# Kernel optimization log

Hardware: AMD Instinct MI355X
Metric: run time of the kernel (lower is better)

The kernel has to match this reference:

```python
import jax, jax.numpy as jnp
import numpy as np

W_CUB = 0.1
W_CD = 1.0
W_EXT = 0.01
W_SPS = 0.01
THRED = 24.0
COS_EPS = 1e-4

# cube face buffers (6 faces x 3 coords)
MASK_PROJECT = jnp.array([[0,1,1],[0,1,1],[1,0,1],[1,0,1],[1,1,0],[1,1,0]], jnp.float32)
MASK_PLANE   = jnp.array([[1,0,0],[1,0,0],[0,1,0],[0,1,0],[0,0,1],[0,0,1]], jnp.float32)
CUBE_NORMAL  = jnp.array([[-1,0,0],[1,0,0],[0,-1,0],[0,1,0],[0,0,-1],[0,0,1]], jnp.float32)
# torch repeat(...,3,...) of [[-1,-1,-1],[1,1,1]] tiles it -> [c0,c1,c0,c1,c0,c1]
CUBE_PLANES6 = jnp.tile(jnp.array([[-1.,-1.,-1.],[1.,1.,1.]], jnp.float32), (3,1))


def setup_inputs():
    B, P, N, S = 4, 24, 3072, 128
    key = jax.random.key(0)
    ks = jax.random.split(key, 8)
    pc_inver = jax.random.normal(ks[0], (B, P, N, 3), jnp.float32)
    normals_inver = jax.random.normal(ks[1], (B, P, N, 3), jnp.float32)
    scale = jax.random.uniform(ks[2], (B, P, 3), jnp.float32) * 0.9 + 0.1
    shape = jax.random.uniform(ks[3], (B, P, 2), jnp.float32) * 1.3 + 0.2
    exist = jax.random.uniform(ks[4], (B, P, 1), jnp.float32) * 0.98 + 0.01
    assign_matrix = jax.nn.softmax(jax.random.normal(ks[5], (B, N, P), jnp.float32), axis=-1)
    etas = jax.random.uniform(ks[6], (B, P, S), jnp.float32, minval=-jnp.pi/2, maxval=jnp.pi/2)
    omegas = jax.random.uniform(ks[7], (B, P, S), jnp.float32, minval=-jnp.pi, maxval=jnp.pi)
    return dict(pc_inver=pc_inver, normals_inver=normals_inver, scale=scale,
                shape=shape, exist=exist, assign_matrix=assign_matrix,
                etas=etas, omegas=omegas)


def _fexp(x, p):
    return jnp.sign(x) * jnp.abs(x) ** p


def _sample_sq_points(scale, eps, etas, omegas):
    # scale (B,P,3), eps (B,P,2), etas/omegas (B,P,S) -> (B,P,S,3)
    etas = jnp.where(etas == 0, 1e-6, etas)
    omegas = jnp.where(omegas == 0, 1e-6, omegas)
    a1, a2, a3 = scale[..., 0:1], scale[..., 1:2], scale[..., 2:3]
    e1, e2 = eps[..., 0:1], eps[..., 1:2]
    ce, se = jnp.cos(etas), jnp.sin(etas)
    co, so = jnp.cos(omegas), jnp.sin(omegas)
    x = a1 * _fexp(ce, e1) * _fexp(co, e2)
    y = a2 * _fexp(ce, e1) * _fexp(so, e2)
    z = a3 * _fexp(se, e1)
    fix = lambda v: (jnp.where(v > 0, 1.0, -1.0)) * jnp.maximum(jnp.abs(v), 1e-6)
    return jnp.stack([fix(x), fix(y), fix(z)], -1)


def _cd_loss(pc_inver, scale, shape, exist, assign_matrix, etas, omegas):
    X = _sample_sq_points(scale, shape, etas, omegas)          # (B,P,S,3)
    diff = X[:, :, :, None, :] - pc_inver[:, :, None, :, :]    # (B,P,S,N,3)
    D = jnp.sum(diff * diff, -1)                               # (B,P,S,N)
    pcl2prim = jnp.min(D, axis=2)                              # (B,P,N)
    pcl_loss = jnp.mean(jnp.sum(jnp.swapaxes(pcl2prim, 1, 2) * assign_matrix, -1))
    prim2pcl = jnp.mean(jnp.min(D, axis=3), axis=-1)           # (B,P)
    e = exist[..., 0]
    prim_loss = jnp.mean(jnp.sum(prim2pcl * e, -1) / (jnp.sum(e, -1) + 1e-6))
    return pcl_loss, prim_loss


def _cuboid_loss(pc_inver, normals_inver, scale, assign_matrix):
    pc = jnp.swapaxes(pc_inver, 1, 2)        # (B,N,P,3)
    nrm = jnp.swapaxes(normals_inver, 1, 2)  # (B,N,P,3)
    n_norm = jnp.maximum(jnp.linalg.norm(nrm, axis=-1, keepdims=True), COS_EPS)
    cos = jnp.einsum('bnpc,fc->bnpf', nrm, CUBE_NORMAL) / n_norm  # ||cube_normal||=1
    idx = jnp.argmax(cos, axis=-1)           # (B,N,P)
    s = scale[:, None, :, None, :]           # (B,1,P,1,3)
    proj = pc[:, :, :, None, :] * MASK_PROJECT + (CUBE_PLANES6 * s) * MASK_PLANE  # (B,N,P,6,3)
    proj = jnp.clip(proj, -s, s)
    proj_sel = jnp.take_along_axis(proj, idx[..., None, None], axis=3)[..., 0, :]  # (B,N,P,3)
    d = jnp.sum((proj_sel - pc) ** 2, -1)    # (B,N,P)
    return jnp.mean(jnp.sum(d * assign_matrix, -1))


def _common_losses(assign_matrix, exist):
    gt = jax.lax.stop_gradient((jnp.sum(assign_matrix, 1) > THRED).astype(jnp.float32))  # (B,P)
    p = exist[..., 0]
    bce = -jnp.mean(gt * jnp.log(p) + (1.0 - gt) * jnp.log1p(-p))
    N = assign_matrix.shape[1]
    sps = jnp.mean(jnp.mean(jnp.sqrt(jnp.sum(assign_matrix, 1) / N + 0.01), -1) ** 2)
    return bce, sps


def reference(pc_inver, normals_inver, scale, shape, exist, assign_matrix, etas, omegas):
    cub = _cuboid_loss(pc_inver, normals_inver, scale, assign_matrix)
    pcl_loss, prim_loss = _cd_loss(pc_inver, scale, shape, exist, assign_matrix, etas, omegas)
    bce, sps = _common_losses(assign_matrix, exist)
    return W_CUB * cub + W_CD * (pcl_loss + prim_loss) + W_EXT * bce + W_SPS * sps
```

## Files before the change

kernel.cpp:

```cpp
#include <hip/hip_runtime.h>
#include <math.h>

#define BB 4
#define PP 24
#define NN 3072
#define SS 128
#define CHUNK 512
#define NSPLIT 6
#define GRID (BB * PP * NSPLIT)
#define FINF 3.4e38f

#define SMIN_F  0
#define SCAL_F  (96 * SS * 8)
#define BPRES_F (SCAL_F + 96 * NSPLIT * 4)
#define CNT_F   (BPRES_F + 96 * 4)

__device__ __forceinline__ float fexp_f(float v, float p) {
    float m = powf(fabsf(v), p);
    float s = (v > 0.f) ? 1.f : ((v < 0.f) ? -1.f : 0.f);
    return s * m;
}
__device__ __forceinline__ float fix_f(float v) {
    return ((v > 0.f) ? 1.f : -1.f) * fmaxf(fabsf(v), 1e-6f);
}
__device__ __forceinline__ float wave_sum(float v) {
    #pragma unroll
    for (int off = 32; off > 0; off >>= 1) v += __shfl_down(v, off);
    return v;
}
__device__ __forceinline__ float aload(const float* p) {
    return __hip_atomic_load(p, __ATOMIC_RELAXED, __HIP_MEMORY_SCOPE_AGENT);
}
__device__ __forceinline__ void astore(float* p, float v) {
    __hip_atomic_store(p, v, __ATOMIC_RELAXED, __HIP_MEMORY_SCOPE_AGENT);
}
__device__ __forceinline__ float cub_dist(float px, float py, float pz,
                                          float nx, float ny, float nz,
                                          float sc0, float sc1, float sc2) {
    float best = -nx; int idx = 0;
    if ( nx > best) { best =  nx; idx = 1; }
    if (-ny > best) { best = -ny; idx = 2; }
    if ( ny > best) { best =  ny; idx = 3; }
    if (-nz > best) { best = -nz; idx = 4; }
    if ( nz > best) { best =  nz; idx = 5; }
    const int c = idx >> 1;
    const float scc = (c == 0) ? sc0 : ((c == 1) ? sc1 : sc2);
    const float fv  = (idx & 1) ? scc : -scc;
    float pr0 = (c == 0) ? fv : fminf(fmaxf(px, -sc0), sc0);
    float pr1 = (c == 1) ? fv : fminf(fmaxf(py, -sc1), sc1);
    float pr2 = (c == 2) ? fv : fminf(fmaxf(pz, -sc2), sc2);
    float d0 = pr0 - px, d1 = pr1 - py, d2 = pr2 - pz;
    return fmaf(d0, d0, fmaf(d1, d1, d2 * d2));
}

__global__ __launch_bounds__(128) void superdec_init(float* __restrict__ ws) {
    const int i = threadIdx.x;
    if (i < 97) ((unsigned*)(ws + CNT_F))[i] = 0u;
}

__global__ __launch_bounds__(256) void superdec_fused(
    const float* __restrict__ pc, const float* __restrict__ nrm,
    const float* __restrict__ scale, const float* __restrict__ shape,
    const float* __restrict__ exist, const float* __restrict__ assign,
    const float* __restrict__ etas, const float* __restrict__ omegas,
    float* __restrict__ ws, float* __restrict__ out)
{
    const int blk   = blockIdx.x;
    const int bp    = blk / NSPLIT;
    const int split = blk % NSPLIT;
    const int b     = bp / PP;
    const int p     = bp % PP;
    const int tid   = threadIdx.x;
    const int n0    = split * CHUNK;
    const int pid   = tid & 127;
    const int q     = tid >> 7;

    __shared__ float4 Xs[SS];
    __shared__ float4 Pts[CHUNK];
    __shared__ float4 dmin2[2][128];
    __shared__ float  red[8 * SS];
    __shared__ float  wsum[6];
    __shared__ unsigned int s_cnt1, s_cnt2;

    const float sc0 = scale[bp * 3 + 0];
    const float sc1 = scale[bp * 3 + 1];
    const float sc2 = scale[bp * 3 + 2];

    const float4* pc4 = (const float4*)(pc + ((size_t)bp * NN + n0) * 3);
    const float4 g0 = pc4[pid * 3 + 0];
    const float4 g1 = pc4[pid * 3 + 1];
    const float4 g2 = pc4[pid * 3 + 2];
    const float px0 = g0.x, py0 = g0.y, pz0 = g0.z;
    const float px1 = g0.w, py1 = g1.x, pz1 = g1.y;
    const float px2 = g1.z, py2 = g1.w, pz2 = g2.x;
    const float px3 = g2.y, py3 = g2.z, pz3 = g2.w;
    const float ps0 = fmaf(px0, px0, fmaf(py0, py0, pz0 * pz0));
    const float ps1 = fmaf(px1, px1, fmaf(py1, py1, pz1 * pz1));
    const float ps2 = fmaf(px2, px2, fmaf(py2, py2, pz2 * pz2));
    const float ps3 = fmaf(px3, px3, fmaf(py3, py3, pz3 * pz3));

    float cub0 = 0.f, cub1 = 0.f, cub2 = 0.f, cub3 = 0.f;
    float am0 = 0.f, am1 = 0.f, am2 = 0.f, am3 = 0.f;

    if (q == 0) {
        {
            const float e1 = shape[bp * 2 + 0];
            const float e2 = shape[bp * 2 + 1];
            float eta = etas[bp * SS + tid];
            float omg = omegas[bp * SS + tid];
            eta = (eta == 0.f) ? 1e-6f : eta;
            omg = (omg == 0.f) ? 1e-6f : omg;
            float ce = cosf(eta), se = sinf(eta);
            float co = cosf(omg), so = sinf(omg);
            float fce = fexp_f(ce, e1);
            float x = fix_f(sc0 * fce * fexp_f(co, e2));
            float y = fix_f(sc1 * fce * fexp_f(so, e2));
            float z = fix_f(sc2 * fexp_f(se, e1));
            float xsq = fmaf(x, x, fmaf(y, y, z * z));
            Xs[tid] = make_float4(-2.f * x, -2.f * y, -2.f * z, xsq);
        }
        Pts[pid * 4 + 0] = make_float4(px0, py0, pz0, ps0);
        Pts[pid * 4 + 1] = make_float4(px1, py1, pz1, ps1);
        Pts[pid * 4 + 2] = make_float4(px2, py2, pz2, ps2);
        Pts[pid * 4 + 3] = make_float4(px3, py3, pz3, ps3);
        const float4* nr4 = (const float4*)(nrm + ((size_t)bp * NN + n0) * 3);
        const float4 h0 = nr4[pid * 3 + 0];
        const float4 h1 = nr4[pid * 3 + 1];
        const float4 h2 = nr4[pid * 3 + 2];
        cub0 = cub_dist(px0, py0, pz0, h0.x, h0.y, h0.z, sc0, sc1, sc2);
        cub1 = cub_dist(px1, py1, pz1, h0.w, h1.x, h1.y, sc0, sc1, sc2);
        cub2 = cub_dist(px2, py2, pz2, h1.z, h1.w, h2.x, sc0, sc1, sc2);
        cub3 = cub_dist(px3, py3, pz3, h2.y, h2.z, h2.w, sc0, sc1, sc2);
        const size_t abase = ((size_t)b * NN + n0 + pid * 4) * PP + p;
        am0 = assign[abase + 0 * PP];
        am1 = assign[abase + 1 * PP];
        am2 = assign[abase + 2 * PP];
        am3 = assign[abase + 3 * PP];
    }
    __syncthreads();

    {
        const int sb = q * 64;
        float m0 = FINF, m1 = FINF, m2 = FINF, m3 = FINF;
        #pragma unroll 4
        for (int s = 0; s < 64; s += 2) {
            float4 xa = Xs[sb + s];
            float4 xb = Xs[sb + s + 1];
            float d;
            d = fmaf(xa.x, px0, fmaf(xa.y, py0, fmaf(xa.z, pz0, xa.w))); m0 = fminf(m0, d);
            d = fmaf(xa.x, px1, fmaf(xa.y, py1, fmaf(xa.z, pz1, xa.w))); m1 = fminf(m1, d);
            d = fmaf(xa.x, px2, fmaf(xa.y, py2, fmaf(xa.z, pz2, xa.w))); m2 = fminf(m2, d);
            d = fmaf(xa.x, px3, fmaf(xa.y, py3, fmaf(xa.z, pz3, xa.w))); m3 = fminf(m3, d);
            d = fmaf(xb.x, px0, fmaf(xb.y, py0, fmaf(xb.z, pz0, xb.w))); m0 = fminf(m0, d);
            d = fmaf(xb.x, px1, fmaf(xb.y, py1, fmaf(xb.z, pz1, xb.w))); m1 = fminf(m1, d);
            d = fmaf(xb.x, px2, fmaf(xb.y, py2, fmaf(xb.z, pz2, xb.w))); m2 = fminf(m2, d);
            d = fmaf(xb.x, px3, fmaf(xb.y, py3, fmaf(xb.z, pz3, xb.w))); m3 = fminf(m3, d);
        }
        dmin2[q][pid] = make_float4(m0, m1, m2, m3);
    }
    __syncthreads();

    if (q == 0) {
        float4 a = dmin2[0][pid];
        float4 c = dmin2[1][pid];
        float d0 = fminf(a.x, c.x) + ps0;
        float d1 = fminf(a.y, c.y) + ps1;
        float d2 = fminf(a.z, c.z) + ps2;
        float d3 = fminf(a.w, c.w) + ps3;
        float acc_pcl = d0 * am0 + d1 * am1 + d2 * am2 + d3 * am3;
        float acc_cub = cub0 * am0 + cub1 * am1 + cub2 * am2 + cub3 * am3;
        float acc_am  = am0 + am1 + am2 + am3;
        float s0 = wave_sum(acc_pcl);
        float s1 = wave_sum(acc_cub);
        float s2 = wave_sum(acc_am);
        const int lane_ = tid & 63, wave = tid >> 6;
        if (lane_ == 0) {
            wsum[wave * 3 + 0] = s0;
            wsum[wave * 3 + 1] = s1;
            wsum[wave * 3 + 2] = s2;
        }
    }

    {
        const int rep = tid >> 5;
        const int sb  = tid & 31;
        const float4 x0 = Xs[sb];
        const float4 x1 = Xs[sb + 32];
        const float4 x2 = Xs[sb + 64];
        const float4 x3 = Xs[sb + 96];
        const int nb = rep * 64;
        float r0 = FINF, r1 = FINF, r2 = FINF, r3 = FINF;
        #pragma unroll 4
        for (int n = 0; n < 64; n += 2) {
            float4 pa = Pts[nb + n];
            float4 pb = Pts[nb + n + 1];
            float d;
            d = fmaf(x0.x, pa.x, fmaf(x0.y, pa.y, fmaf(x0.z, pa.z, pa.w))); r0 = fminf(r0, d);
            d = fmaf(x1.x, pa.x, fmaf(x1.y, pa.y, fmaf(x1.z, pa.z, pa.w))); r1 = fminf(r1, d);
            d = fmaf(x2.x, pa.x, fmaf(x2.y, pa.y, fmaf(x2.z, pa.z, pa.w))); r2 = fminf(r2, d);
            d = fmaf(x3.x, pa.x, fmaf(x3.y, pa.y, fmaf(x3.z, pa.z, pa.w))); r3 = fminf(r3, d);
            d = fmaf(x0.x, pb.x, fmaf(x0.y, pb.y, fmaf(x0.z, pb.z, pb.w))); r0 = fminf(r0, d);
            d = fmaf(x1.x, pb.x, fmaf(x1.y, pb.y, fmaf(x1.z, pb.z, pb.w))); r1 = fminf(r1, d);
            d = fmaf(x2.x, pb.x, fmaf(x2.y, pb.y, fmaf(x2.z, pb.z, pb.w))); r2 = fminf(r2, d);
            d = fmaf(x3.x, pb.x, fmaf(x3.y, pb.y, fmaf(x3.z, pb.z, pb.w))); r3 = fminf(r3, d);
        }
        red[rep * SS + sb +  0] = r0;
        red[rep * SS + sb + 32] = r1;
        red[rep * SS + sb + 64] = r2;
        red[rep * SS + sb + 96] = r3;
    }
    __syncthreads();

    if (tid < SS) {
        float m = red[tid];
        #pragma unroll
        for (int r = 1; r < 8; ++r) m = fminf(m, red[r * SS + tid]);
        astore(ws + SMIN_F + ((bp * SS + tid) << 3) + split, m + Xs[tid].w);
    }
    if (tid == 0) {
        float* sc = ws + SCAL_F + (bp * NSPLIT + split) * 4;
        astore(sc + 0, wsum[0] + wsum[3]);
        astore(sc + 1, wsum[1] + wsum[4]);
        astore(sc + 2, wsum[2] + wsum[5]);
    }

    __syncthreads();
    if (tid == 0) {
        asm volatile("s_waitcnt vmcnt(0)" ::: "memory");
        s_cnt1 = __hip_atomic_fetch_add((unsigned*)(ws + CNT_F) + bp, 1u,
                                        __ATOMIC_RELAXED, __HIP_MEMORY_SCOPE_AGENT);
    }
    __syncthreads();
    if (s_cnt1 != (unsigned)(NSPLIT - 1)) return;

    {
        const int lane = tid & 63;
        if (tid < SS) {
            const float* mb = ws + SMIN_F + ((bp * SS + tid) << 3);
            const float v0 = aload(mb + 0), v1 = aload(mb + 1), v2 = aload(mb + 2);
            const float v3 = aload(mb + 3), v4 = aload(mb + 4), v5 = aload(mb + 5);
            float m = fminf(fminf(fminf(v0, v1), fminf(v2, v3)), fminf(v4, v5));
            float sm = wave_sum(m);
            if (lane == 0) wsum[tid >> 6] = sm;
        } else if (tid < 128 + 18) {
            const int j = tid - 128, sp = j / 3, c = j % 3;
            red[600 + j] = aload(ws + SCAL_F + (bp * NSPLIT + sp) * 4 + c);
        }
        __syncthreads();
        if (tid == 0) {
            const float prim = wsum[0] + wsum[1];
            float pcl = 0.f, cubv = 0.f, cs = 0.f;
            #pragma unroll
            for (int sp = 0; sp < NSPLIT; ++sp) {
                pcl  += red[600 + sp * 3 + 0];
                cubv += red[600 + sp * 3 + 1];
                cs   += red[600 + sp * 3 + 2];
            }
            float* r4 = ws + BPRES_F + bp * 4;
            astore(r4 + 0, prim);
            astore(r4 + 1, pcl);
            astore(r4 + 2, cubv);
            astore(r4 + 3, cs);
            asm volatile("s_waitcnt vmcnt(0)" ::: "memory");
            s_cnt2 = __hip_atomic_fetch_add((unsigned*)(ws + CNT_F) + 96, 1u,
                                            __ATOMIC_RELAXED, __HIP_MEMORY_SCOPE_AGENT);
        }
        __syncthreads();
        if (s_cnt2 != 95u) return;
    }

    if (tid < 96) {
        const float* r4 = ws + BPRES_F + tid * 4;
        const float prim = aload(r4 + 0);
        const float pcl  = aload(r4 + 1);
        const float cubv = aload(r4 + 2);
        const float cs   = aload(r4 + 3);
        const float e  = exist[tid];
        const float gt = (cs > 24.0f) ? 1.f : 0.f;
        red[  0 + tid] = prim;
        red[ 96 + tid] = pcl;
        red[192 + tid] = cubv;
        red[288 + tid] = gt * logf(e) + (1.f - gt) * log1pf(-e);
        red[384 + tid] = e;
        red[480 + tid] = sqrtf(cs / (float)NN + 0.01f);
    }
    __syncthreads();

    if (tid == 0) {
        float pcl_sum = 0.f, cub_sum = 0.f, bce_sum = 0.f, prim_loss = 0.f, sps = 0.f;
        #pragma unroll
        for (int b_ = 0; b_ < BB; ++b_) {
            float pe = 0.f, ee = 0.f, sq = 0.f;
            #pragma unroll
            for (int p_ = 0; p_ < PP; ++p_) {
                const int i = b_ * PP + p_;
                pcl_sum += red[ 96 + i];
                cub_sum += red[192 + i];
                bce_sum += red[288 + i];
                pe += (red[i] / (float)SS) * red[384 + i];
                ee += red[384 + i];
                sq += red[480 + i];
            }
            prim_loss += pe / (ee + 1e-6f);
            float mb = sq / (float)PP;
            sps += mb * mb;
        }
        prim_loss /= (float)BB;
        sps       /= (float)BB;
        float pcl_loss = pcl_sum / (float)(BB * NN);
        float cubf     = cub_sum / (float)(BB * NN);
        float bce      = -bce_sum / (float)(BB * PP);
        out[0] = 0.1f * cubf + 1.0f * (pcl_loss + prim_loss) + 0.01f * bce + 0.01f * sps;
    }
}

extern "C" void kernel_launch(void* const* d_in, const int* in_sizes, int n_in,
                              void* d_out, int out_size, void* d_ws, size_t ws_size,
                              hipStream_t stream) {
    const float* pc     = (const float*)d_in[0];
    const float* nrm    = (const float*)d_in[1];
    const float* scale  = (const float*)d_in[2];
    const float* shape  = (const float*)d_in[3];
    const float* exist  = (const float*)d_in[4];
    const float* assign = (const float*)d_in[5];
    const float* etas   = (const float*)d_in[6];
    const float* omegas = (const float*)d_in[7];
    float* ws  = (float*)d_ws;
    float* out = (float*)d_out;

    superdec_init<<<1, 128, 0, stream>>>(ws);

    superdec_fused<<<GRID, 256, 0, stream>>>(
        pc, nrm, scale, shape, exist, assign, etas, omegas, ws, out);
}
```

Before: 89.23 us.

## Compute each distance once for both Chamfer directions in a fused tile pass

```diff
diff --git a/kernel.cpp b/kernel.cpp
--- a/kernel.cpp
+++ b/kernel.cpp
@@ -72,160 +72,169 @@
     const int p     = bp % PP;
     const int tid   = threadIdx.x;
     const int n0    = split * CHUNK;
-    const int pid   = tid & 127;
-    const int q     = tid >> 7;
+    const int pg    = tid & 63;
+    const int sg    = tid >> 6;
 
     __shared__ float4 Xs[SS];
-    __shared__ float4 Pts[CHUNK];
-    __shared__ float4 dmin2[2][128];
-    __shared__ float  red[8 * SS];
+    __shared__ float  s_red[4][32][68];
+    __shared__ float4 dminL[4][64][2];
+    __shared__ float4 cubam[128][2];
+    __shared__ float  red[1024];
     __shared__ float  wsum[6];
-    __shared__ unsigned int s_cnt1, s_cnt2;
+    __shared__ unsigned s_cnt1, s_cnt2;
 
     const float sc0 = scale[bp * 3 + 0];
     const float sc1 = scale[bp * 3 + 1];
     const float sc2 = scale[bp * 3 + 2];
 
     const float4* pc4 = (const float4*)(pc + ((size_t)bp * NN + n0) * 3);
-    const float4 g0 = pc4[pid * 3 + 0];
-    const float4 g1 = pc4[pid * 3 + 1];
-    const float4 g2 = pc4[pid * 3 + 2];
-    const float px0 = g0.x, py0 = g0.y, pz0 = g0.z;
-    const float px1 = g0.w, py1 = g1.x, pz1 = g1.y;
-    const float px2 = g1.z, py2 = g1.w, pz2 = g2.x;
-    const float px3 = g2.y, py3 = g2.z, pz3 = g2.w;
-    const float ps0 = fmaf(px0, px0, fmaf(py0, py0, pz0 * pz0));
-    const float ps1 = fmaf(px1, px1, fmaf(py1, py1, pz1 * pz1));
-    const float ps2 = fmaf(px2, px2, fmaf(py2, py2, pz2 * pz2));
-    const float ps3 = fmaf(px3, px3, fmaf(py3, py3, pz3 * pz3));
-
-    float cub0 = 0.f, cub1 = 0.f, cub2 = 0.f, cub3 = 0.f;
-    float am0 = 0.f, am1 = 0.f, am2 = 0.f, am3 = 0.f;
-
-    if (q == 0) {
-        {
-            const float e1 = shape[bp * 2 + 0];
-            const float e2 = shape[bp * 2 + 1];
-            float eta = etas[bp * SS + tid];
-            float omg = omegas[bp * SS + tid];
-            eta = (eta == 0.f) ? 1e-6f : eta;
-            omg = (omg == 0.f) ? 1e-6f : omg;
-            float ce = cosf(eta), se = sinf(eta);
-            float co = cosf(omg), so = sinf(omg);
-            float fce = fexp_f(ce, e1);
-            float x = fix_f(sc0 * fce * fexp_f(co, e2));
-            float y = fix_f(sc1 * fce * fexp_f(so, e2));
-            float z = fix_f(sc2 * fexp_f(se, e1));
-            float xsq = fmaf(x, x, fmaf(y, y, z * z));
-            Xs[tid] = make_float4(-2.f * x, -2.f * y, -2.f * z, xsq);
-        }
-        Pts[pid * 4 + 0] = make_float4(px0, py0, pz0, ps0);
-        Pts[pid * 4 + 1] = make_float4(px1, py1, pz1, ps1);
-        Pts[pid * 4 + 2] = make_float4(px2, py2, pz2, ps2);
-        Pts[pid * 4 + 3] = make_float4(px3, py3, pz3, ps3);
+    float px[8], py[8], pz[8], psq[8];
+    {
+        const float4 g0 = pc4[pg * 6 + 0];
+        const float4 g1 = pc4[pg * 6 + 1];
+        const float4 g2 = pc4[pg * 6 + 2];
+        const float4 g3 = pc4[pg * 6 + 3];
+        const float4 g4 = pc4[pg * 6 + 4];
+        const float4 g5 = pc4[pg * 6 + 5];
+        px[0]=g0.x; py[0]=g0.y; pz[0]=g0.z;
+        px[1]=g0.w; py[1]=g1.x; pz[1]=g1.y;
+        px[2]=g1.z; py[2]=g1.w; pz[2]=g2.x;
+        px[3]=g2.y; py[3]=g2.z; pz[3]=g2.w;
+        px[4]=g3.x; py[4]=g3.y; pz[4]=g3.z;
+        px[5]=g3.w; py[5]=g4.x; pz[5]=g4.y;
+        px[6]=g4.z; py[6]=g4.w; pz[6]=g5.x;
+        px[7]=g5.y; py[7]=g5.z; pz[7]=g5.w;
+        #pragma unroll
+        for (int j = 0; j < 8; ++j)
+            psq[j] = fmaf(px[j], px[j], fmaf(py[j], py[j], pz[j] * pz[j]));
+    }
+
+    const int pid = tid & 127;
+    const float4 a0 = pc4[pid * 3 + 0];
+    const float4 a1 = pc4[pid * 3 + 1];
+    const float4 a2 = pc4[pid * 3 + 2];
+    const float qx0 = a0.x, qy0 = a0.y, qz0 = a0.z;
+    const float qx1 = a0.w, qy1 = a1.x, qz1 = a1.y;
+    const float qx2 = a1.z, qy2 = a1.w, qz2 = a2.x;
+    const float qx3 = a2.y, qy3 = a2.z, qz3 = a2.w;
+    const float qs0 = fmaf(qx0, qx0, fmaf(qy0, qy0, qz0 * qz0));
+    const float qs1 = fmaf(qx1, qx1, fmaf(qy1, qy1, qz1 * qz1));
+    const float qs2 = fmaf(qx2, qx2, fmaf(qy2, qy2, qz2 * qz2));
+    const float qs3 = fmaf(qx3, qx3, fmaf(qy3, qy3, qz3 * qz3));
+
+    if (tid < 128) {
+        const float e1 = shape[bp * 2 + 0];
+        const float e2 = shape[bp * 2 + 1];
+        float eta = etas[bp * SS + tid];
+        float omg = omegas[bp * SS + tid];
+        eta = (eta == 0.f) ? 1e-6f : eta;
+        omg = (omg == 0.f) ? 1e-6f : omg;
+        float ce = cosf(eta), se = sinf(eta);
+        float co = cosf(omg), so = sinf(omg);
+        float fce = fexp_f(ce, e1);
+        float x = fix_f(sc0 * fce * fexp_f(co, e2));
+        float y = fix_f(sc1 * fce * fexp_f(so, e2));
+        float z = fix_f(sc2 * fexp_f(se, e1));
+        float xsq = fmaf(x, x, fmaf(y, y, z * z));
+        Xs[tid] = make_float4(-2.f * x, -2.f * y, -2.f * z, xsq);
+    } else {
         const float4* nr4 = (const float4*)(nrm + ((size_t)bp * NN + n0) * 3);
         const float4 h0 = nr4[pid * 3 + 0];
         const float4 h1 = nr4[pid * 3 + 1];
         const float4 h2 = nr4[pid * 3 + 2];
-        cub0 = cub_dist(px0, py0, pz0, h0.x, h0.y, h0.z, sc0, sc1, sc2);
-        cub1 = cub_dist(px1, py1, pz1, h0.w, h1.x, h1.y, sc0, sc1, sc2);
-        cub2 = cub_dist(px2, py2, pz2, h1.z, h1.w, h2.x, sc0, sc1, sc2);
-        cub3 = cub_dist(px3, py3, pz3, h2.y, h2.z, h2.w, sc0, sc1, sc2);
+        float c0 = cub_dist(qx0, qy0, qz0, h0.x, h0.y, h0.z, sc0, sc1, sc2);
+        float c1 = cub_dist(qx1, qy1, qz1, h0.w, h1.x, h1.y, sc0, sc1, sc2);
+        float c2 = cub_dist(qx2, qy2, qz2, h1.z, h1.w, h2.x, sc0, sc1, sc2);
+        float c3 = cub_dist(qx3, qy3, qz3, h2.y, h2.z, h2.w, sc0, sc1, sc2);
         const size_t abase = ((size_t)b * NN + n0 + pid * 4) * PP + p;
-        am0 = assign[abase + 0 * PP];
-        am1 = assign[abase + 1 * PP];
-        am2 = assign[abase + 2 * PP];
-        am3 = assign[abase + 3 * PP];
+        const float m0 = assign[abase + 0 * PP];
+        const float m1 = assign[abase + 1 * PP];
+        const float m2 = assign[abase + 2 * PP];
+        const float m3 = assign[abase + 3 * PP];
+        cubam[pid][0] = make_float4(c0, c1, c2, c3);
+        cubam[pid][1] = make_float4(m0, m1, m2, m3);
     }
     __syncthreads();
 
     {
-        const int sb = q * 64;
-        float m0 = FINF, m1 = FINF, m2 = FINF, m3 = FINF;
+        float pmin[8];
+        #pragma unroll
+        for (int j = 0; j < 8; ++j) pmin[j] = FINF;
+        const int sb = sg * 32;
         #pragma unroll 4
-        for (int s = 0; s < 64; s += 2) {
-            float4 xa = Xs[sb + s];
-            float4 xb = Xs[sb + s + 1];
-            float d;
-            d = fmaf(xa.x, px0, fmaf(xa.y, py0, fmaf(xa.z, pz0, xa.w))); m0 = fminf(m0, d);
-            d = fmaf(xa.x, px1, fmaf(xa.y, py1, fmaf(xa.z, pz1, xa.w))); m1 = fminf(m1, d);
-            d = fmaf(xa.x, px2, fmaf(xa.y, py2, fmaf(xa.z, pz2, xa.w))); m2 = fminf(m2, d);
-            d = fmaf(xa.x, px3, fmaf(xa.y, py3, fmaf(xa.z, pz3, xa.w))); m3 = fminf(m3, d);
-            d = fmaf(xb.x, px0, fmaf(xb.y, py0, fmaf(xb.z, pz0, xb.w))); m0 = fminf(m0, d);
-            d = fmaf(xb.x, px1, fmaf(xb.y, py1, fmaf(xb.z, pz1, xb.w))); m1 = fminf(m1, d);
-            d = fmaf(xb.x, px2, fmaf(xb.y, py2, fmaf(xb.z, pz2, xb.w))); m2 = fminf(m2, d);
-            d = fmaf(xb.x, px3, fmaf(xb.y, py3, fmaf(xb.z, pz3, xb.w))); m3 = fminf(m3, d);
-        }
-        dmin2[q][pid] = make_float4(m0, m1, m2, m3);
-    }
-    __syncthreads();
-
-    if (q == 0) {
-        float4 a = dmin2[0][pid];
-        float4 c = dmin2[1][pid];
-        float d0 = fminf(a.x, c.x) + ps0;
-        float d1 = fminf(a.y, c.y) + ps1;
-        float d2 = fminf(a.z, c.z) + ps2;
-        float d3 = fminf(a.w, c.w) + ps3;
-        float acc_pcl = d0 * am0 + d1 * am1 + d2 * am2 + d3 * am3;
-        float acc_cub = cub0 * am0 + cub1 * am1 + cub2 * am2 + cub3 * am3;
-        float acc_am  = am0 + am1 + am2 + am3;
-        float s0 = wave_sum(acc_pcl);
-        float s1 = wave_sum(acc_cub);
-        float s2 = wave_sum(acc_am);
-        const int lane_ = tid & 63, wave = tid >> 6;
+        for (int k = 0; k < 32; ++k) {
+            const float4 x = Xs[sb + k];
+            float d0 = fmaf(x.x, px[0], fmaf(x.y, py[0], fmaf(x.z, pz[0], x.w)));
+            float d1 = fmaf(x.x, px[1], fmaf(x.y, py[1], fmaf(x.z, pz[1], x.w)));
+            float d2 = fmaf(x.x, px[2], fmaf(x.y, py[2], fmaf(x.z, pz[2], x.w)));
+            float d3 = fmaf(x.x, px[3], fmaf(x.y, py[3], fmaf(x.z, pz[3], x.w)));
+            float d4 = fmaf(x.x, px[4], fmaf(x.y, py[4], fmaf(x.z, pz[4], x.w)));
+            float d5 = fmaf(x.x, px[5], fmaf(x.y, py[5], fmaf(x.z, pz[5], x.w)));
+            float d6 = fmaf(x.x, px[6], fmaf(x.y, py[6], fmaf(x.z, pz[6], x.w)));
+            float d7 = fmaf(x.x, px[7], fmaf(x.y, py[7], fmaf(x.z, pz[7], x.w)));
+            pmin[0] = fminf(pmin[0], d0);
+            pmin[1] = fminf(pmin[1], d1);
+            pmin[2] = fminf(pmin[2], d2);
+            pmin[3] = fminf(pmin[3], d3);
+            pmin[4] = fminf(pmin[4], d4);
+            pmin[5] = fminf(pmin[5], d5);
+            pmin[6] = fminf(pmin[6], d6);
+            pmin[7] = fminf(pmin[7], d7);
+            const float e0 = d0 + psq[0], e1 = d1 + psq[1];
+            const float e2 = d2 + psq[2], e3 = d3 + psq[3];
+            const float e4 = d4 + psq[4], e5 = d5 + psq[5];
+            const float e6 = d6 + psq[6], e7 = d7 + psq[7];
+            const float sv = fminf(fminf(fminf(e0, e1), fminf(e2, e3)),
+                                   fminf(fminf(e4, e5), fminf(e6, e7)));
+            s_red[sg][k][pg] = sv;
+        }
+        dminL[sg][pg][0] = make_float4(pmin[0], pmin[1], pmin[2], pmin[3]);
+        dminL[sg][pg][1] = make_float4(pmin[4], pmin[5], pmin[6], pmin[7]);
+    }
+    __syncthreads();
+
+    if (tid < SS) {
+        const int zg = tid >> 5, k = tid & 31;
+        const float4* r4 = (const float4*)&s_red[zg][k][0];
+        float m = FINF;
+        #pragma unroll
+        for (int i = 0; i < 16; ++i) {
+            const float4 v = r4[i];
+            m = fminf(fminf(fminf(m, v.x), v.y), fminf(v.z, v.w));
+        }
+        astore(ws + SMIN_F + ((bp * SS + tid) << 3) + split, m);
+
+        const int pg2 = tid >> 1, hf = tid & 1;
+        const float4 e0 = dminL[0][pg2][hf];
+        const float4 e1 = dminL[1][pg2][hf];
+        const float4 e2 = dminL[2][pg2][hf];
+        const float4 e3 = dminL[3][pg2][hf];
+        const float dd0 = fminf(fminf(e0.x, e1.x), fminf(e2.x, e3.x)) + qs0;
+        const float dd1 = fminf(fminf(e0.y, e1.y), fminf(e2.y, e3.y)) + qs1;
+        const float dd2 = fminf(fminf(e0.z, e1.z), fminf(e2.z, e3.z)) + qs2;
+        const float dd3 = fminf(fminf(e0.w, e1.w), fminf(e2.w, e3.w)) + qs3;
+        const float4 cb = cubam[tid][0];
+        const float4 am = cubam[tid][1];
+        const float acc_pcl = dd0 * am.x + dd1 * am.y + dd2 * am.z + dd3 * am.w;
+        const float acc_cub = cb.x * am.x + cb.y * am.y + cb.z * am.z + cb.w * am.w;
+        const float acc_am  = am.x + am.y + am.z + am.w;
+        const float s0 = wave_sum(acc_pcl);
+        const float s1 = wave_sum(acc_cub);
+        const float s2 = wave_sum(acc_am);
+        const int lane_ = tid & 63, wv = tid >> 6;
         if (lane_ == 0) {
-            wsum[wave * 3 + 0] = s0;
-            wsum[wave * 3 + 1] = s1;
-            wsum[wave * 3 + 2] = s2;
-        }
-    }
-
-    {
-        const int rep = tid >> 5;
-        const int sb  = tid & 31;
-        const float4 x0 = Xs[sb];
-        const float4 x1 = Xs[sb + 32];
-        const float4 x2 = Xs[sb + 64];
-        const float4 x3 = Xs[sb + 96];
-        const int nb = rep * 64;
-        float r0 = FINF, r1 = FINF, r2 = FINF, r3 = FINF;
-        #pragma unroll 4
-        for (int n = 0; n < 64; n += 2) {
-            float4 pa = Pts[nb + n];
-            float4 pb = Pts[nb + n + 1];
-            float d;
-            d = fmaf(x0.x, pa.x, fmaf(x0.y, pa.y, fmaf(x0.z, pa.z, pa.w))); r0 = fminf(r0, d);
-            d = fmaf(x1.x, pa.x, fmaf(x1.y, pa.y, fmaf(x1.z, pa.z, pa.w))); r1 = fminf(r1, d);
-            d = fmaf(x2.x, pa.x, fmaf(x2.y, pa.y, fmaf(x2.z, pa.z, pa.w))); r2 = fminf(r2, d);
-            d = fmaf(x3.x, pa.x, fmaf(x3.y, pa.y, fmaf(x3.z, pa.z, pa.w))); r3 = fminf(r3, d);
-            d = fmaf(x0.x, pb.x, fmaf(x0.y, pb.y, fmaf(x0.z, pb.z, pb.w))); r0 = fminf(r0, d);
-            d = fmaf(x1.x, pb.x, fmaf(x1.y, pb.y, fmaf(x1.z, pb.z, pb.w))); r1 = fminf(r1, d);
-            d = fmaf(x2.x, pb.x, fmaf(x2.y, pb.y, fmaf(x2.z, pb.z, pb.w))); r2 = fminf(r2, d);
-            d = fmaf(x3.x, pb.x, fmaf(x3.y, pb.y, fmaf(x3.z, pb.z, pb.w))); r3 = fminf(r3, d);
-        }
-        red[rep * SS + sb +  0] = r0;
-        red[rep * SS + sb + 32] = r1;
-        red[rep * SS + sb + 64] = r2;
-        red[rep * SS + sb + 96] = r3;
-    }
-    __syncthreads();
-
-    if (tid < SS) {
-        float m = red[tid];
-        #pragma unroll
-        for (int r = 1; r < 8; ++r) m = fminf(m, red[r * SS + tid]);
-        astore(ws + SMIN_F + ((bp * SS + tid) << 3) + split, m + Xs[tid].w);
-    }
+            wsum[wv * 3 + 0] = s0;
+            wsum[wv * 3 + 1] = s1;
+            wsum[wv * 3 + 2] = s2;
+        }
+    }
+
+    __syncthreads();
     if (tid == 0) {
         float* sc = ws + SCAL_F + (bp * NSPLIT + split) * 4;
         astore(sc + 0, wsum[0] + wsum[3]);
         astore(sc + 1, wsum[1] + wsum[4]);
         astore(sc + 2, wsum[2] + wsum[5]);
-    }
-
-    __syncthreads();
-    if (tid == 0) {
         asm volatile("s_waitcnt vmcnt(0)" ::: "memory");
         s_cnt1 = __hip_atomic_fetch_add((unsigned*)(ws + CNT_F) + bp, 1u,
                                         __ATOMIC_RELAXED, __HIP_MEMORY_SCOPE_AGENT);
```

Result: no change. 89.61 us (+0.4%).
